# Performance work log

Measured on AMD Instinct MI355X. Metric: run time of the kernel, lower is better.

## Reference

```python
import jax, jax.numpy as jnp
import numpy as np

C_IN = 256
K = 4
C_QK = C_IN // K  # 64


def setup_inputs() -> dict:
    key = jax.random.key(0)
    ks = jax.random.split(key, 9)
    B, C, H, W = 4, C_IN, 64, 64
    s = 0.02
    return {
        "x": jax.random.normal(ks[0], (B, C, H, W), dtype=jnp.float32),
        # 1x1 convs stored as dense [out, in] matrices (kernel_size=1)
        "wq": jax.random.normal(ks[1], (C_QK, C), dtype=jnp.float32) * s,
        "bq": jax.random.normal(ks[2], (C_QK,), dtype=jnp.float32) * s,
        "wk": jax.random.normal(ks[3], (C_QK, C), dtype=jnp.float32) * s,
        "bk": jax.random.normal(ks[4], (C_QK,), dtype=jnp.float32) * s,
        "wv": jax.random.normal(ks[5], (C, C), dtype=jnp.float32) * s,
        "bv": jax.random.normal(ks[6], (C,), dtype=jnp.float32) * s,
        "wg": jax.random.normal(ks[7], (C, C), dtype=jnp.float32) * s,
        "bg": jax.random.normal(ks[8], (C,), dtype=jnp.float32) * s,
    }


def reference(x, wq, bq, wk, bk, wv, bv, wg, bg):
    B, C, H, W = x.shape
    N = H * W
    xf = x.reshape(B, C, N)  # [B, C, N]
    # 1x1 conv == per-pixel linear over channels
    q = jnp.einsum("oc,bcn->bon", wq, xf) + bq[None, :, None]  # [B, Cqk, N]
    k = jnp.einsum("oc,bcn->bon", wk, xf) + bk[None, :, None]  # [B, Cqk, N]
    v = jnp.einsum("oc,bcn->bon", wv, xf) + bv[None, :, None]  # [B, C, N]
    # energy[b, n, m] = <q[:, n], k[:, m]>  (n = query pos, m = key pos)
    energy = jnp.einsum("bon,bom->bnm", q, k)  # [B, N, N]
    energy = jax.nn.elu(energy) / N
    # out[b, c, m] = sum_n v[b, c, n] * energy[b, n, m]
    out = jnp.einsum("bcn,bnm->bcm", v, energy).reshape(B, C, H, W)
    out = jnp.einsum("oc,bchw->bohw", wg, out) + bg[None, :, None, None]
    return out
```

## Files before the change

### kernel.cpp

```cpp
#include <hip/hip_runtime.h>

#define B_ 4
#define C_ 256
#define CQK 64
#define N_ 4096
#define SEG 2
#define SEGN (N_ / SEG)
#define NB 128
#define ITERS (SEGN / NB)
#define TS 512

typedef _Float16 f16;
typedef __attribute__((ext_vector_type(8))) _Float16 f16x8;
typedef __attribute__((ext_vector_type(4))) _Float16 f16x4;
typedef __attribute__((ext_vector_type(4))) float f32x4;
typedef __attribute__((ext_vector_type(4))) float float4v;

#define TILE_OFF(l15, quad) ((l15) * 32 + (quad) * 8)

__global__ __launch_bounds__(256) void prep_w(
    const float* __restrict__ wq, const float* __restrict__ wk,
    const float* __restrict__ wv, const float* __restrict__ wg,
    f16* __restrict__ WQt, f16* __restrict__ WKt, f16* __restrict__ WVt,
    f16* __restrict__ WGt) {
  int chunk = blockIdx.x * 256 + threadIdx.x;
  if (chunk >= 20480) return;
  const float* src;
  f16* dst;
  int lo;
  if (chunk < 2048) { src = wq; dst = WQt; lo = chunk * 8; }
  else if (chunk < 4096) { src = wk; dst = WKt; lo = (chunk - 2048) * 8; }
  else if (chunk < 12288) { src = wv; dst = WVt; lo = (chunk - 4096) * 8; }
  else { src = wg; dst = WGt; lo = (chunk - 12288) * 8; }
  int o = lo >> 8, k = lo & 255;
  f16x8 v;
#pragma unroll
  for (int j = 0; j < 8; j++) v[j] = (f16)src[lo + j];
  *(f16x8*)(dst + ((size_t)(o >> 4) * 8 + (k >> 5)) * TS + (o & 15) * 32 + (k & 31)) = v;
}

__global__ __launch_bounds__(512) void proj(
    const float* __restrict__ x, const f16* __restrict__ WQt,
    const f16* __restrict__ WKt, const f16* __restrict__ WVt,
    const float* __restrict__ bq, const float* __restrict__ bk,
    const float* __restrict__ bv, f16* __restrict__ QTt, f16* __restrict__ KTt,
    f16* __restrict__ Vt) {
  __shared__ float xs[64][65];
  __shared__ f16 xt[4 * 8 * TS];
  int n0 = blockIdx.x * 64;
  int b = blockIdx.y;
  int tid = threadIdx.x, lane = tid & 63, w = tid >> 6;
  int l15 = lane & 15, quad = lane >> 4;
  const float* xb = x + (size_t)b * C_ * N_;

  for (int cc = 0; cc < 4; cc++) {
#pragma unroll
    for (int i = 0; i < 8; i++)
      xs[lane][w * 8 + i] = xb[(size_t)(cc * 64 + w * 8 + i) * N_ + n0 + lane];
    __syncthreads();
    {
      int nt = w >> 1;
      f16x8 v;
#pragma unroll
      for (int j = 0; j < 8; j++)
        v[j] = (f16)xs[nt * 16 + l15][32 * (w & 1) + quad * 8 + j];
      *(f16x8*)(xt + (nt * 8 + cc * 2 + (w & 1)) * TS + l15 * 32 + quad * 8) = v;
    }
    __syncthreads();
  }

  f32x4 acc[3][4];
#pragma unroll
  for (int j = 0; j < 3; j++)
#pragma unroll
    for (int nt = 0; nt < 4; nt++) acc[j][nt] = (f32x4){0.f, 0.f, 0.f, 0.f};

#pragma unroll
  for (int kt = 0; kt < 8; kt++) {
    f16x8 xf[4];
#pragma unroll
    for (int nt = 0; nt < 4; nt++)
      xf[nt] = *(const f16x8*)(xt + (nt * 8 + kt) * TS + TILE_OFF(l15, quad));
#pragma unroll
    for (int j = 0; j < 3; j++) {
      int g = w * 3 + j;
      const f16* Wt;
      int ot;
      bool isV = g < 16;
      if (isV) { Wt = WVt; ot = g; }
      else if (g < 20) { Wt = WQt; ot = g - 16; }
      else { Wt = WKt; ot = g - 20; }
      f16x8 wf = *(const f16x8*)(Wt + ((size_t)ot * 8 + kt) * TS + TILE_OFF(l15, quad));
#pragma unroll
      for (int nt = 0; nt < 4; nt++)
        acc[j][nt] = isV
            ? __builtin_amdgcn_mfma_f32_16x16x32_f16(xf[nt], wf, acc[j][nt], 0, 0, 0)
            : __builtin_amdgcn_mfma_f32_16x16x32_f16(wf, xf[nt], acc[j][nt], 0, 0, 0);
    }
  }

  f16* vbout = Vt + (size_t)b * C_ * N_;
#pragma unroll
  for (int j = 0; j < 3; j++) {
    int g = w * 3 + j;
    if (g < 16) {
      float bvv = bv[16 * g + l15];
#pragma unroll
      for (int nt = 0; nt < 4; nt++) {
        f16x4 vals;
#pragma unroll
        for (int r = 0; r < 4; r++) vals[r] = (f16)(acc[j][nt][r] + bvv);
        *(f16x4*)(vbout + ((size_t)g * 128 + (n0 >> 5) + (nt >> 1)) * TS +
                  l15 * 32 + 16 * (nt & 1) + 4 * quad) = vals;
      }
    } else {
      int oq = (g < 20) ? (g - 16) : (g - 20);
      const float* bias = (g < 20) ? bq : bk;
      f16* ob = ((g < 20) ? QTt : KTt) + (size_t)b * N_ * CQK;
#pragma unroll
      for (int nt = 0; nt < 4; nt++) {
        f16x4 vals;
#pragma unroll
        for (int r = 0; r < 4; r++)
          vals[r] = (f16)(acc[j][nt][r] + bias[16 * oq + 4 * quad + r]);
        *(f16x4*)(ob + (((size_t)(n0 >> 4) + nt) * 2 + (oq >> 1)) * TS + l15 * 32 +
                  16 * (oq & 1) + 4 * quad) = vals;
      }
    }
  }
}

__global__ __launch_bounds__(256, 2) void attn(const f16* __restrict__ qt,
                                               const f16* __restrict__ kt,
                                               const f16* __restrict__ v,
                                               const f16* __restrict__ WGt,
                                               f16* __restrict__ part) {
  __shared__ __align__(16) f16 sPt[2][64][128];
  int sb = blockIdx.x;
  int seg = sb >> 2;
  int b = sb & 3;
  int m0 = blockIdx.y * 64;
  int tid = threadIdx.x, lane = tid & 63, w = tid >> 6;
  int l15 = lane & 15, quad = lane >> 4;
  const f16* qtb = qt + (size_t)b * N_ * CQK;
  const f16* ktb = kt + (size_t)b * N_ * CQK;
  const f16* vb = v + (size_t)b * C_ * N_;

  f32x4 oacc[4][4];
#pragma unroll
  for (int ct = 0; ct < 4; ct++)
#pragma unroll
    for (int mt = 0; mt < 4; mt++) oacc[ct][mt] = (f32x4){0.f, 0.f, 0.f, 0.f};

  f16x8 kf[4][2];
#pragma unroll
  for (int mt = 0; mt < 4; mt++)
#pragma unroll
    for (int ks = 0; ks < 2; ks++)
      kf[mt][ks] = *(const f16x8*)(ktb + ((size_t)((m0 >> 4) + mt) * 2 + ks) * TS +
                                   TILE_OFF(l15, quad));

  f16x8 qf[2][2];
  {
    int nq = seg * SEGN;
#pragma unroll
    for (int nt = 0; nt < 2; nt++)
#pragma unroll
      for (int ks = 0; ks < 2; ks++)
        qf[nt][ks] = *(const f16x8*)(qtb +
                                     ((size_t)((nq >> 4) + 2 * w + nt) * 2 + ks) * TS +
                                     TILE_OFF(l15, quad));
  }

  for (int it = 0; it < ITERS; it++) {
    int n0 = seg * SEGN + it * NB;
    f16x8 vfA[2][4];
#pragma unroll
    for (int ks = 0; ks < 2; ks++)
#pragma unroll
      for (int ct = 0; ct < 4; ct++)
        vfA[ks][ct] = *(const f16x8*)(vb +
                                      ((size_t)(4 * w + ct) * 128 + (n0 >> 5) + ks) * TS +
                                      TILE_OFF(l15, quad));

    char* buf = (char*)sPt[it & 1];
#pragma unroll
    for (int nt = 0; nt < 2; nt++) {
      f32x4 sacc[4];
#pragma unroll
      for (int mt = 0; mt < 4; mt++) sacc[mt] = (f32x4){0.f, 0.f, 0.f, 0.f};
#pragma unroll
      for (int ks = 0; ks < 2; ks++)
#pragma unroll
        for (int mt = 0; mt < 4; mt++)
          sacc[mt] = __builtin_amdgcn_mfma_f32_16x16x32_f16(qf[nt][ks], kf[mt][ks],
                                                            sacc[mt], 0, 0, 0);
#pragma unroll
      for (int mt = 0; mt < 4; mt++) {
        f16x4 p;
#pragma unroll
        for (int r = 0; r < 4; r++) {
          float s = sacc[mt][r];
          p[r] = (f16)(s > 0.0f ? s : (__expf(s) - 1.0f));
        }
        int row = 16 * mt + l15;
        int colb = (64 * w + 32 * nt + 8 * quad) ^ ((row & 7) << 4);
        *(f16x4*)(buf + row * 256 + colb) = p;
      }
    }
    __syncthreads();

    f16x8 vfB[2][4];
    f16x8 pa[4];
#pragma unroll
    for (int mt = 0; mt < 4; mt++) {
      int row = 16 * mt + l15;
      pa[mt] = *(const f16x8*)(buf + row * 256 + ((quad * 16) ^ ((row & 7) << 4)));
    }
#pragma unroll
    for (int ks = 0; ks < 2; ks++)
#pragma unroll
      for (int ct = 0; ct < 4; ct++)
        vfB[ks][ct] = *(const f16x8*)(vb + ((size_t)(4 * w + ct) * 128 + (n0 >> 5) +
                                            2 + ks) * TS +
                                      TILE_OFF(l15, quad));
#pragma unroll
    for (int ct = 0; ct < 4; ct++)
#pragma unroll
      for (int mt = 0; mt < 4; mt++)
        oacc[ct][mt] = __builtin_amdgcn_mfma_f32_16x16x32_f16(vfA[0][ct], pa[mt],
                                                              oacc[ct][mt], 0, 0, 0);
    if (it + 1 < ITERS) {
      int nq = n0 + NB;
#pragma unroll
      for (int nt = 0; nt < 2; nt++)
#pragma unroll
        for (int ks = 0; ks < 2; ks++)
          qf[nt][ks] = *(const f16x8*)(qtb +
                                       ((size_t)((nq >> 4) + 2 * w + nt) * 2 + ks) * TS +
                                       TILE_OFF(l15, quad));
    }
#pragma unroll
    for (int mt = 0; mt < 4; mt++) {
      int row = 16 * mt + l15;
      pa[mt] = *(const f16x8*)(buf + row * 256 + ((64 + quad * 16) ^ ((row & 7) << 4)));
    }
#pragma unroll
    for (int ct = 0; ct < 4; ct++)
#pragma unroll
      for (int mt = 0; mt < 4; mt++)
        oacc[ct][mt] = __builtin_amdgcn_mfma_f32_16x16x32_f16(vfA[1][ct], pa[mt],
                                                              oacc[ct][mt], 0, 0, 0);
#pragma unroll
    for (int mt = 0; mt < 4; mt++) {
      int row = 16 * mt + l15;
      pa[mt] = *(const f16x8*)(buf + row * 256 + ((128 + quad * 16) ^ ((row & 7) << 4)));
    }
#pragma unroll
    for (int ct = 0; ct < 4; ct++)
#pragma unroll
      for (int mt = 0; mt < 4; mt++)
        oacc[ct][mt] = __builtin_amdgcn_mfma_f32_16x16x32_f16(vfB[0][ct], pa[mt],
                                                              oacc[ct][mt], 0, 0, 0);
#pragma unroll
    for (int mt = 0; mt < 4; mt++) {
      int row = 16 * mt + l15;
      pa[mt] = *(const f16x8*)(buf + row * 256 + ((192 + quad * 16) ^ ((row & 7) << 4)));
    }
#pragma unroll
    for (int ct = 0; ct < 4; ct++)
#pragma unroll
      for (int mt = 0; mt < 4; mt++)
        oacc[ct][mt] = __builtin_amdgcn_mfma_f32_16x16x32_f16(vfB[1][ct], pa[mt],
                                                              oacc[ct][mt], 0, 0, 0);
  }

  __syncthreads();
  f16* obuf = (f16*)sPt;
#pragma unroll
  for (int ct = 0; ct < 4; ct++) {
#pragma unroll
    for (int mt = 0; mt < 4; mt++) {
      f16x4 vals;
#pragma unroll
      for (int r = 0; r < 4; r++)
        vals[r] = (f16)(oacc[ct][mt][r] * (1.0f / (float)N_));
      *(f16x4*)(obuf + (mt * 8 + 2 * w + (ct >> 1)) * TS + l15 * 32 +
                16 * (ct & 1) + 4 * quad) = vals;
    }
  }
  __syncthreads();
  f32x4 accO[4][4];
#pragma unroll
  for (int ot = 0; ot < 4; ot++)
#pragma unroll
    for (int mt = 0; mt < 4; mt++) accO[ot][mt] = (f32x4){0.f, 0.f, 0.f, 0.f};
#pragma unroll
  for (int kt = 0; kt < 8; kt++) {
    f16x8 bO[4];
#pragma unroll
    for (int mt = 0; mt < 4; mt++)
      bO[mt] = *(const f16x8*)(obuf + (mt * 8 + kt) * TS + TILE_OFF(l15, quad));
#pragma unroll
    for (int ot = 0; ot < 4; ot++) {
      f16x8 af = *(const f16x8*)(WGt + ((size_t)(4 * w + ot) * 8 + kt) * TS +
                                 TILE_OFF(l15, quad));
#pragma unroll
      for (int mt = 0; mt < 4; mt++)
        accO[ot][mt] = __builtin_amdgcn_mfma_f32_16x16x32_f16(af, bO[mt], accO[ot][mt], 0, 0, 0);
    }
  }
  f16* pb = part + ((size_t)(seg * B_ + b) * C_) * N_;
#pragma unroll
  for (int ot = 0; ot < 4; ot++) {
#pragma unroll
    for (int mt = 0; mt < 4; mt++) {
      int m = m0 + 16 * mt + l15;
#pragma unroll
      for (int r = 0; r < 4; r++) {
        int o = 64 * w + 16 * ot + 4 * quad + r;
        pb[(size_t)o * N_ + m] = (f16)accO[ot][mt][r];
      }
    }
  }
}

__global__ __launch_bounds__(256) void combine(const f16* __restrict__ part,
                                               const float* __restrict__ bg,
                                               float* __restrict__ out) {
  size_t i = ((size_t)blockIdx.x * 256 + threadIdx.x) * 8;
  f16x8 p0 = *(const f16x8*)(part + i);
  f16x8 p1 = *(const f16x8*)(part + (size_t)B_ * C_ * N_ + i);
  float bgo = bg[(i >> 12) & 255];
  float4v r0, r1;
#pragma unroll
  for (int j = 0; j < 4; j++) r0[j] = (float)p0[j] + (float)p1[j] + bgo;
#pragma unroll
  for (int j = 0; j < 4; j++) r1[j] = (float)p0[4 + j] + (float)p1[4 + j] + bgo;
  *(float4v*)(out + i) = r0;
  *(float4v*)(out + i + 4) = r1;
}

extern "C" void kernel_launch(void* const* d_in, const int* in_sizes, int n_in,
                              void* d_out, int out_size, void* d_ws, size_t ws_size,
                              hipStream_t stream) {
  const float* x = (const float*)d_in[0];
  const float* wq = (const float*)d_in[1];
  const float* bq = (const float*)d_in[2];
  const float* wk = (const float*)d_in[3];
  const float* bk = (const float*)d_in[4];
  const float* wv = (const float*)d_in[5];
  const float* bv = (const float*)d_in[6];
  const float* wg = (const float*)d_in[7];
  const float* bg = (const float*)d_in[8];
  float* out = (float*)d_out;

  char* ws = (char*)d_ws;
  f16* QTt = (f16*)ws; ws += (size_t)B_ * N_ * CQK * sizeof(f16);
  f16* KTt = (f16*)ws; ws += (size_t)B_ * N_ * CQK * sizeof(f16);
  f16* Vt  = (f16*)ws; ws += (size_t)B_ * C_ * N_ * sizeof(f16);
  f16* WQt = (f16*)ws; ws += (size_t)CQK * C_ * sizeof(f16);
  f16* WKt = (f16*)ws; ws += (size_t)CQK * C_ * sizeof(f16);
  f16* WVt = (f16*)ws; ws += (size_t)C_ * C_ * sizeof(f16);
  f16* WGt = (f16*)ws; ws += (size_t)C_ * C_ * sizeof(f16);
  f16* PART = (f16*)ws; ws += (size_t)SEG * B_ * C_ * N_ * sizeof(f16);

  prep_w<<<dim3(80), 256, 0, stream>>>(wq, wk, wv, wg, WQt, WKt, WVt, WGt);
  proj<<<dim3(N_ / 64, B_), 512, 0, stream>>>(x, WQt, WKt, WVt, bq, bk, bv,
                                              QTt, KTt, Vt);
  attn<<<dim3(8, N_ / 64), 256, 0, stream>>>(QTt, KTt, Vt, WGt, PART);
  combine<<<dim3(2048), 256, 0, stream>>>(PART, bg, out);
}
```

Measured before the change: 160.5 us.

## Split attention block across 8 waves and stage K tile in LDS

The attention kernel now runs with 512 threads (8 waves) per block instead of 256. Each wave handles 16 query rows and 32 channels rather than 32 and 64, which halves per-wave accumulators and register fragments, and launch bounds are raised to target 4 blocks per SM. The K fragments are loaded once into shared memory and re-read from LDS each iteration, where before they were held in registers. This adds LDS traffic and more waves contending at each barrier, in exchange for higher occupancy to hide memory latency.

```diff
diff --git a/kernel.cpp b/kernel.cpp
--- a/kernel.cpp
+++ b/kernel.cpp
@@ -130,11 +130,12 @@
   }
 }
 
-__global__ __launch_bounds__(256, 2) void attn(const f16* __restrict__ qt,
+__global__ __launch_bounds__(512, 4) void attn(const f16* __restrict__ qt,
                                                const f16* __restrict__ kt,
                                                const f16* __restrict__ v,
                                                const f16* __restrict__ WGt,
                                                f16* __restrict__ part) {
+  __shared__ __align__(16) f16 sK[8 * TS];
   __shared__ __align__(16) f16 sPt[2][64][128];
   int sb = blockIdx.x;
   int seg = sb >> 2;
@@ -146,110 +147,98 @@
   const f16* ktb = kt + (size_t)b * N_ * CQK;
   const f16* vb = v + (size_t)b * C_ * N_;
 
-  f32x4 oacc[4][4];
-#pragma unroll
-  for (int ct = 0; ct < 4; ct++)
+  *(f16x8*)(sK + w * TS + TILE_OFF(l15, quad)) =
+      *(const f16x8*)(ktb + ((size_t)((m0 >> 4) + (w >> 1)) * 2 + (w & 1)) * TS +
+                      TILE_OFF(l15, quad));
+
+  f32x4 oacc[2][4];
+#pragma unroll
+  for (int ct = 0; ct < 2; ct++)
 #pragma unroll
     for (int mt = 0; mt < 4; mt++) oacc[ct][mt] = (f32x4){0.f, 0.f, 0.f, 0.f};
 
-  f16x8 kf[4][2];
-#pragma unroll
-  for (int mt = 0; mt < 4; mt++)
-#pragma unroll
-    for (int ks = 0; ks < 2; ks++)
-      kf[mt][ks] = *(const f16x8*)(ktb + ((size_t)((m0 >> 4) + mt) * 2 + ks) * TS +
-                                   TILE_OFF(l15, quad));
-
-  f16x8 qf[2][2];
-  {
-    int nq = seg * SEGN;
-#pragma unroll
-    for (int nt = 0; nt < 2; nt++)
-#pragma unroll
-      for (int ks = 0; ks < 2; ks++)
-        qf[nt][ks] = *(const f16x8*)(qtb +
-                                     ((size_t)((nq >> 4) + 2 * w + nt) * 2 + ks) * TS +
-                                     TILE_OFF(l15, quad));
-  }
+  f16x8 qf[2];
+#pragma unroll
+  for (int ks = 0; ks < 2; ks++)
+    qf[ks] = *(const f16x8*)(qtb + ((size_t)(((seg * SEGN) >> 4) + w) * 2 + ks) * TS +
+                             TILE_OFF(l15, quad));
+
+  __syncthreads();
 
   for (int it = 0; it < ITERS; it++) {
     int n0 = seg * SEGN + it * NB;
-    f16x8 vfA[2][4];
-#pragma unroll
-    for (int ks = 0; ks < 2; ks++)
-#pragma unroll
-      for (int ct = 0; ct < 4; ct++)
-        vfA[ks][ct] = *(const f16x8*)(vb +
-                                      ((size_t)(4 * w + ct) * 128 + (n0 >> 5) + ks) * TS +
-                                      TILE_OFF(l15, quad));
-
     char* buf = (char*)sPt[it & 1];
-#pragma unroll
-    for (int nt = 0; nt < 2; nt++) {
-      f32x4 sacc[4];
-#pragma unroll
-      for (int mt = 0; mt < 4; mt++) sacc[mt] = (f32x4){0.f, 0.f, 0.f, 0.f};
-#pragma unroll
-      for (int ks = 0; ks < 2; ks++)
-#pragma unroll
-        for (int mt = 0; mt < 4; mt++)
-          sacc[mt] = __builtin_amdgcn_mfma_f32_16x16x32_f16(qf[nt][ks], kf[mt][ks],
-                                                            sacc[mt], 0, 0, 0);
-#pragma unroll
-      for (int mt = 0; mt < 4; mt++) {
-        f16x4 p;
-#pragma unroll
-        for (int r = 0; r < 4; r++) {
-          float s = sacc[mt][r];
-          p[r] = (f16)(s > 0.0f ? s : (__expf(s) - 1.0f));
-        }
-        int row = 16 * mt + l15;
-        int colb = (64 * w + 32 * nt + 8 * quad) ^ ((row & 7) << 4);
-        *(f16x4*)(buf + row * 256 + colb) = p;
+
+    f32x4 sacc[4];
+#pragma unroll
+    for (int mt = 0; mt < 4; mt++) sacc[mt] = (f32x4){0.f, 0.f, 0.f, 0.f};
+#pragma unroll
+    for (int ks = 0; ks < 2; ks++) {
+      f16x8 kf[4];
+#pragma unroll
+      for (int mt = 0; mt < 4; mt++)
+        kf[mt] = *(const f16x8*)(sK + (mt * 2 + ks) * TS + TILE_OFF(l15, quad));
+#pragma unroll
+      for (int mt = 0; mt < 4; mt++)
+        sacc[mt] = __builtin_amdgcn_mfma_f32_16x16x32_f16(qf[ks], kf[mt], sacc[mt],
+                                                          0, 0, 0);
+    }
+#pragma unroll
+    for (int mt = 0; mt < 4; mt++) {
+      f16x4 p;
+#pragma unroll
+      for (int r = 0; r < 4; r++) {
+        float s = sacc[mt][r];
+        p[r] = (f16)(s > 0.0f ? s : (__expf(s) - 1.0f));
       }
+      int row = 16 * mt + l15;
+      int colb = (32 * w + 8 * quad) ^ ((row & 7) << 4);
+      *(f16x4*)(buf + row * 256 + colb) = p;
     }
     __syncthreads();
 
-    f16x8 vfB[2][4];
-    f16x8 pa[4];
-#pragma unroll
-    for (int mt = 0; mt < 4; mt++) {
-      int row = 16 * mt + l15;
-      pa[mt] = *(const f16x8*)(buf + row * 256 + ((quad * 16) ^ ((row & 7) << 4)));
-    }
-#pragma unroll
-    for (int ks = 0; ks < 2; ks++)
-#pragma unroll
-      for (int ct = 0; ct < 4; ct++)
-        vfB[ks][ct] = *(const f16x8*)(vb + ((size_t)(4 * w + ct) * 128 + (n0 >> 5) +
-                                            2 + ks) * TS +
-                                      TILE_OFF(l15, quad));
-#pragma unroll
-    for (int ct = 0; ct < 4; ct++)
-#pragma unroll
-      for (int mt = 0; mt < 4; mt++)
-        oacc[ct][mt] = __builtin_amdgcn_mfma_f32_16x16x32_f16(vfA[0][ct], pa[mt],
-                                                              oacc[ct][mt], 0, 0, 0);
     if (it + 1 < ITERS) {
       int nq = n0 + NB;
 #pragma unroll
-      for (int nt = 0; nt < 2; nt++)
-#pragma unroll
-        for (int ks = 0; ks < 2; ks++)
-          qf[nt][ks] = *(const f16x8*)(qtb +
-                                       ((size_t)((nq >> 4) + 2 * w + nt) * 2 + ks) * TS +
-                                       TILE_OFF(l15, quad));
-    }
+      for (int ks = 0; ks < 2; ks++)
+        qf[ks] = *(const f16x8*)(qtb + ((size_t)((nq >> 4) + w) * 2 + ks) * TS +
+                                 TILE_OFF(l15, quad));
+    }
+
+    f16x8 vfa[2], vfb[2], pa[4];
+#pragma unroll
+    for (int ct = 0; ct < 2; ct++)
+      vfa[ct] = *(const f16x8*)(vb + ((size_t)(2 * w + ct) * 128 + (n0 >> 5) + 0) * TS +
+                                TILE_OFF(l15, quad));
+#pragma unroll
+    for (int mt = 0; mt < 4; mt++) {
+      int row = 16 * mt + l15;
+      pa[mt] = *(const f16x8*)(buf + row * 256 + ((0 + quad * 16) ^ ((row & 7) << 4)));
+    }
+#pragma unroll
+    for (int ct = 0; ct < 2; ct++)
+      vfb[ct] = *(const f16x8*)(vb + ((size_t)(2 * w + ct) * 128 + (n0 >> 5) + 1) * TS +
+                                TILE_OFF(l15, quad));
+#pragma unroll
+    for (int ct = 0; ct < 2; ct++)
+#pragma unroll
+      for (int mt = 0; mt < 4; mt++)
+        oacc[ct][mt] = __builtin_amdgcn_mfma_f32_16x16x32_f16(vfa[ct], pa[mt],
+                                                              oacc[ct][mt], 0, 0, 0);
 #pragma unroll
     for (int mt = 0; mt < 4; mt++) {
       int row = 16 * mt + l15;
       pa[mt] = *(const f16x8*)(buf + row * 256 + ((64 + quad * 16) ^ ((row & 7) << 4)));
     }
 #pragma unroll
-    for (int ct = 0; ct < 4; ct++)
-#pragma unroll
-      for (int mt = 0; mt < 4; mt++)
-        oacc[ct][mt] = __builtin_amdgcn_mfma_f32_16x16x32_f16(vfA[1][ct], pa[mt],
+    for (int ct = 0; ct < 2; ct++)
+      vfa[ct] = *(const f16x8*)(vb + ((size_t)(2 * w + ct) * 128 + (n0 >> 5) + 2) * TS +
+                                TILE_OFF(l15, quad));
+#pragma unroll
+    for (int ct = 0; ct < 2; ct++)
+#pragma unroll
+      for (int mt = 0; mt < 4; mt++)
+        oacc[ct][mt] = __builtin_amdgcn_mfma_f32_16x16x32_f16(vfb[ct], pa[mt],
                                                               oacc[ct][mt], 0, 0, 0);
 #pragma unroll
     for (int mt = 0; mt < 4; mt++) {
@@ -257,10 +246,14 @@
       pa[mt] = *(const f16x8*)(buf + row * 256 + ((128 + quad * 16) ^ ((row & 7) << 4)));
     }
 #pragma unroll
-    for (int ct = 0; ct < 4; ct++)
-#pragma unroll
-      for (int mt = 0; mt < 4; mt++)
-        oacc[ct][mt] = __builtin_amdgcn_mfma_f32_16x16x32_f16(vfB[0][ct], pa[mt],
+    for (int ct = 0; ct < 2; ct++)
+      vfb[ct] = *(const f16x8*)(vb + ((size_t)(2 * w + ct) * 128 + (n0 >> 5) + 3) * TS +
+                                TILE_OFF(l15, quad));
+#pragma unroll
+    for (int ct = 0; ct < 2; ct++)
+#pragma unroll
+      for (int mt = 0; mt < 4; mt++)
+        oacc[ct][mt] = __builtin_amdgcn_mfma_f32_16x16x32_f16(vfa[ct], pa[mt],
                                                               oacc[ct][mt], 0, 0, 0);
 #pragma unroll
     for (int mt = 0; mt < 4; mt++) {
@@ -268,31 +261,30 @@
       pa[mt] = *(const f16x8*)(buf + row * 256 + ((192 + quad * 16) ^ ((row & 7) << 4)));
     }
 #pragma unroll
-    for (int ct = 0; ct < 4; ct++)
-#pragma unroll
-      for (int mt = 0; mt < 4; mt++)
-        oacc[ct][mt] = __builtin_amdgcn_mfma_f32_16x16x32_f16(vfB[1][ct], pa[mt],
+    for (int ct = 0; ct < 2; ct++)
+#pragma unroll
+      for (int mt = 0; mt < 4; mt++)
+        oacc[ct][mt] = __builtin_amdgcn_mfma_f32_16x16x32_f16(vfb[ct], pa[mt],
                                                               oacc[ct][mt], 0, 0, 0);
   }
 
   __syncthreads();
   f16* obuf = (f16*)sPt;
 #pragma unroll
-  for (int ct = 0; ct < 4; ct++) {
+  for (int ct = 0; ct < 2; ct++) {
 #pragma unroll
     for (int mt = 0; mt < 4; mt++) {
       f16x4 vals;
 #pragma unroll
       for (int r = 0; r < 4; r++)
         vals[r] = (f16)(oacc[ct][mt][r] * (1.0f / (float)N_));
-      *(f16x4*)(obuf + (mt * 8 + 2 * w + (ct >> 1)) * TS + l15 * 32 +
-                16 * (ct & 1) + 4 * quad) = vals;
+      *(f16x4*)(obuf + (mt * 8 + w) * TS + l15 * 32 + 16 * ct + 4 * quad) = vals;
     }
   }
   __syncthreads();
-  f32x4 accO[4][4];
-#pragma unroll
-  for (int ot = 0; ot < 4; ot++)
+  f32x4 accO[2][4];
+#pragma unroll
+  for (int ot = 0; ot < 2; ot++)
 #pragma unroll
     for (int mt = 0; mt < 4; mt++) accO[ot][mt] = (f32x4){0.f, 0.f, 0.f, 0.f};
 #pragma unroll
@@ -302,23 +294,24 @@
     for (int mt = 0; mt < 4; mt++)
       bO[mt] = *(const f16x8*)(obuf + (mt * 8 + kt) * TS + TILE_OFF(l15, quad));
 #pragma unroll
-    for (int ot = 0; ot < 4; ot++) {
-      f16x8 af = *(const f16x8*)(WGt + ((size_t)(4 * w + ot) * 8 + kt) * TS +
+    for (int ot = 0; ot < 2; ot++) {
+      f16x8 af = *(const f16x8*)(WGt + ((size_t)(2 * w + ot) * 8 + kt) * TS +
                                  TILE_OFF(l15, quad));
 #pragma unroll
       for (int mt = 0; mt < 4; mt++)
-        accO[ot][mt] = __builtin_amdgcn_mfma_f32_16x16x32_f16(af, bO[mt], accO[ot][mt], 0, 0, 0);
+        accO[ot][mt] = __builtin_amdgcn_mfma_f32_16x16x32_f16(af, bO[mt], accO[ot][mt],
+                                                              0, 0, 0);
     }
   }
   f16* pb = part + ((size_t)(seg * B_ + b) * C_) * N_;
 #pragma unroll
-  for (int ot = 0; ot < 4; ot++) {
+  for (int ot = 0; ot < 2; ot++) {
 #pragma unroll
     for (int mt = 0; mt < 4; mt++) {
       int m = m0 + 16 * mt + l15;
 #pragma unroll
       for (int r = 0; r < 4; r++) {
-        int o = 64 * w + 16 * ot + 4 * quad + r;
+        int o = 32 * w + 16 * ot + 4 * quad + r;
         pb[(size_t)o * N_ + m] = (f16)accO[ot][mt][r];
       }
     }
@@ -368,6 +361,6 @@
   prep_w<<<dim3(80), 256, 0, stream>>>(wq, wk, wv, wg, WQt, WKt, WVt, WGt);
   proj<<<dim3(N_ / 64, B_), 512, 0, stream>>>(x, WQt, WKt, WVt, bq, bk, bv,
                                               QTt, KTt, Vt);
-  attn<<<dim3(8, N_ / 64), 256, 0, stream>>>(QTt, KTt, Vt, WGt, PART);
+  attn<<<dim3(SEG * B_, N_ / 64), 512, 0, stream>>>(QTt, KTt, Vt, WGt, PART);
   combine<<<dim3(2048), 256, 0, stream>>>(PART, bg, out);
 }
```

Result: no change. 160.4 us (-0.0%).

## Fuse split-N combine into attention via float atomics and stagger iteration order

Applied to the files above, without the earlier changes.

Drops the fp16 partial buffer and the separate combine kernel. Each attention block now atomically adds its fp32 projected result, plus half the bias, straight into the zeroed output. It also rotates the starting N-iteration per block so concurrent blocks read different V/Q tiles and spread cache and channel traffic. This trades a write-and-reread of partials and one launch for a memset and scattered, uncoalesced atomic adds.

```diff
diff --git a/kernel.cpp b/kernel.cpp
--- a/kernel.cpp
+++ b/kernel.cpp
@@ -134,12 +134,14 @@
                                                const f16* __restrict__ kt,
                                                const f16* __restrict__ v,
                                                const f16* __restrict__ WGt,
-                                               f16* __restrict__ part) {
+                                               const float* __restrict__ bg,
+                                               float* __restrict__ out) {
   __shared__ __align__(16) f16 sPt[2][64][128];
   int sb = blockIdx.x;
   int seg = sb >> 2;
   int b = sb & 3;
   int m0 = blockIdx.y * 64;
+  int it0 = ((((int)blockIdx.y >> 5) << 3) ^ (((int)blockIdx.y & 7) << 1)) & (ITERS - 1);
   int tid = threadIdx.x, lane = tid & 63, w = tid >> 6;
   int l15 = lane & 15, quad = lane >> 4;
   const f16* qtb = qt + (size_t)b * N_ * CQK;
@@ -162,7 +164,7 @@
 
   f16x8 qf[2][2];
   {
-    int nq = seg * SEGN;
+    int nq = seg * SEGN + it0 * NB;
 #pragma unroll
     for (int nt = 0; nt < 2; nt++)
 #pragma unroll
@@ -172,7 +174,8 @@
                                      TILE_OFF(l15, quad));
   }
 
-  for (int it = 0; it < ITERS; it++) {
+  for (int i = 0; i < ITERS; i++) {
+    int it = (i + it0) & (ITERS - 1);
     int n0 = seg * SEGN + it * NB;
     f16x8 vfA[2][4];
 #pragma unroll
@@ -183,7 +186,7 @@
                                       ((size_t)(4 * w + ct) * 128 + (n0 >> 5) + ks) * TS +
                                       TILE_OFF(l15, quad));
 
-    char* buf = (char*)sPt[it & 1];
+    char* buf = (char*)sPt[i & 1];
 #pragma unroll
     for (int nt = 0; nt < 2; nt++) {
       f32x4 sacc[4];
@@ -230,8 +233,9 @@
       for (int mt = 0; mt < 4; mt++)
         oacc[ct][mt] = __builtin_amdgcn_mfma_f32_16x16x32_f16(vfA[0][ct], pa[mt],
                                                               oacc[ct][mt], 0, 0, 0);
-    if (it + 1 < ITERS) {
-      int nq = n0 + NB;
+    if (i + 1 < ITERS) {
+      int itn = (i + 1 + it0) & (ITERS - 1);
+      int nq = seg * SEGN + itn * NB;
 #pragma unroll
       for (int nt = 0; nt < 2; nt++)
 #pragma unroll
@@ -310,35 +314,21 @@
         accO[ot][mt] = __builtin_amdgcn_mfma_f32_16x16x32_f16(af, bO[mt], accO[ot][mt], 0, 0, 0);
     }
   }
-  f16* pb = part + ((size_t)(seg * B_ + b) * C_) * N_;
+  float* ob = out + (size_t)b * C_ * N_;
 #pragma unroll
   for (int ot = 0; ot < 4; ot++) {
+    float4v bgq = *(const float4v*)(bg + 64 * w + 16 * ot + 4 * quad);
 #pragma unroll
     for (int mt = 0; mt < 4; mt++) {
       int m = m0 + 16 * mt + l15;
 #pragma unroll
       for (int r = 0; r < 4; r++) {
         int o = 64 * w + 16 * ot + 4 * quad + r;
-        pb[(size_t)o * N_ + m] = (f16)accO[ot][mt][r];
+        atomicAdd(&ob[(size_t)o * N_ + m],
+                  accO[ot][mt][r] + bgq[r] * (1.0f / (float)SEG));
       }
     }
   }
-}
-
-__global__ __launch_bounds__(256) void combine(const f16* __restrict__ part,
-                                               const float* __restrict__ bg,
-                                               float* __restrict__ out) {
-  size_t i = ((size_t)blockIdx.x * 256 + threadIdx.x) * 8;
-  f16x8 p0 = *(const f16x8*)(part + i);
-  f16x8 p1 = *(const f16x8*)(part + (size_t)B_ * C_ * N_ + i);
-  float bgo = bg[(i >> 12) & 255];
-  float4v r0, r1;
-#pragma unroll
-  for (int j = 0; j < 4; j++) r0[j] = (float)p0[j] + (float)p1[j] + bgo;
-#pragma unroll
-  for (int j = 0; j < 4; j++) r1[j] = (float)p0[4 + j] + (float)p1[4 + j] + bgo;
-  *(float4v*)(out + i) = r0;
-  *(float4v*)(out + i + 4) = r1;
 }
 
 extern "C" void kernel_launch(void* const* d_in, const int* in_sizes, int n_in,
@@ -363,11 +353,10 @@
   f16* WKt = (f16*)ws; ws += (size_t)CQK * C_ * sizeof(f16);
   f16* WVt = (f16*)ws; ws += (size_t)C_ * C_ * sizeof(f16);
   f16* WGt = (f16*)ws; ws += (size_t)C_ * C_ * sizeof(f16);
-  f16* PART = (f16*)ws; ws += (size_t)SEG * B_ * C_ * N_ * sizeof(f16);
-
+
+  hipMemsetAsync(out, 0, out_size, stream);
   prep_w<<<dim3(80), 256, 0, stream>>>(wq, wk, wv, wg, WQt, WKt, WVt, WGt);
   proj<<<dim3(N_ / 64, B_), 512, 0, stream>>>(x, WQt, WKt, WVt, bq, bk, bv,
                                               QTt, KTt, Vt);
-  attn<<<dim3(8, N_ / 64), 256, 0, stream>>>(QTt, KTt, Vt, WGt, PART);
-  combine<<<dim3(2048), 256, 0, stream>>>(PART, bg, out);
+  attn<<<dim3(SEG * B_, N_ / 64), 256, 0, stream>>>(QTt, KTt, Vt, WGt, bg, out);
 }
```

Measured after the change: 171.7 us. 7.0% more time.

## Software-pipeline attention: compute next tile's ELU scores during current PV MFMAs

Applied to the files above, without the earlier changes.

Restructures the attention loop so the QK^T score MFMAs and ELU for the next key block are interleaved with the PV accumulation MFMAs of the current block, writing into the alternate LDS buffer. A prologue computes the first score tile, and the single barrier per iteration moves to the loop end. This targets the serialization between score computation, the barrier and the PV matmul, at the cost of extra live registers (s0/s1) that may reduce occupancy or cause spills.

```diff
diff --git a/kernel.cpp b/kernel.cpp
--- a/kernel.cpp
+++ b/kernel.cpp
@@ -161,29 +161,16 @@
                                    TILE_OFF(l15, quad));
 
   f16x8 qf[2][2];
+#pragma unroll
+  for (int nt = 0; nt < 2; nt++)
+#pragma unroll
+    for (int ks = 0; ks < 2; ks++)
+      qf[nt][ks] = *(const f16x8*)(qtb +
+                                   ((size_t)(((seg * SEGN) >> 4) + 2 * w + nt) * 2 + ks) * TS +
+                                   TILE_OFF(l15, quad));
+
   {
-    int nq = seg * SEGN;
-#pragma unroll
-    for (int nt = 0; nt < 2; nt++)
-#pragma unroll
-      for (int ks = 0; ks < 2; ks++)
-        qf[nt][ks] = *(const f16x8*)(qtb +
-                                     ((size_t)((nq >> 4) + 2 * w + nt) * 2 + ks) * TS +
-                                     TILE_OFF(l15, quad));
-  }
-
-  for (int it = 0; it < ITERS; it++) {
-    int n0 = seg * SEGN + it * NB;
-    f16x8 vfA[2][4];
-#pragma unroll
-    for (int ks = 0; ks < 2; ks++)
-#pragma unroll
-      for (int ct = 0; ct < 4; ct++)
-        vfA[ks][ct] = *(const f16x8*)(vb +
-                                      ((size_t)(4 * w + ct) * 128 + (n0 >> 5) + ks) * TS +
-                                      TILE_OFF(l15, quad));
-
-    char* buf = (char*)sPt[it & 1];
+    char* buf = (char*)sPt[0];
 #pragma unroll
     for (int nt = 0; nt < 2; nt++) {
       f32x4 sacc[4];
@@ -208,15 +195,60 @@
         *(f16x4*)(buf + row * 256 + colb) = p;
       }
     }
-    __syncthreads();
+  }
+  {
+    int nq = seg * SEGN + NB;
+#pragma unroll
+    for (int nt = 0; nt < 2; nt++)
+#pragma unroll
+      for (int ks = 0; ks < 2; ks++)
+        qf[nt][ks] = *(const f16x8*)(qtb +
+                                     ((size_t)((nq >> 4) + 2 * w + nt) * 2 + ks) * TS +
+                                     TILE_OFF(l15, quad));
+  }
+  __syncthreads();
+
+  for (int it = 0; it < ITERS; it++) {
+    int n0 = seg * SEGN + it * NB;
+    char* rbuf = (char*)sPt[it & 1];
+    char* wbuf = (char*)sPt[(it + 1) & 1];
+    bool hasNext = (it + 1 < ITERS);
+
+    f16x8 vfA[2][4];
+#pragma unroll
+    for (int ks = 0; ks < 2; ks++)
+#pragma unroll
+      for (int ct = 0; ct < 4; ct++)
+        vfA[ks][ct] = *(const f16x8*)(vb +
+                                      ((size_t)(4 * w + ct) * 128 + (n0 >> 5) + ks) * TS +
+                                      TILE_OFF(l15, quad));
+
+    f32x4 s0[4], s1[4];
+    if (hasNext) {
+#pragma unroll
+      for (int mt = 0; mt < 4; mt++) s0[mt] = (f32x4){0.f, 0.f, 0.f, 0.f};
+#pragma unroll
+      for (int ks = 0; ks < 2; ks++)
+#pragma unroll
+        for (int mt = 0; mt < 4; mt++)
+          s0[mt] = __builtin_amdgcn_mfma_f32_16x16x32_f16(qf[0][ks], kf[mt][ks],
+                                                          s0[mt], 0, 0, 0);
+    }
+
+    f16x8 pa[4];
+#pragma unroll
+    for (int mt = 0; mt < 4; mt++) {
+      int row = 16 * mt + l15;
+      pa[mt] = *(const f16x8*)(rbuf + row * 256 + ((quad * 16) ^ ((row & 7) << 4)));
+    }
+#pragma unroll
+    for (int ct = 0; ct < 4; ct++)
+#pragma unroll
+      for (int mt = 0; mt < 4; mt++)
+        oacc[ct][mt] = __builtin_amdgcn_mfma_f32_16x16x32_f16(vfA[0][ct], pa[mt],
+                                                              oacc[ct][mt], 0, 0, 0);
 
     f16x8 vfB[2][4];
-    f16x8 pa[4];
-#pragma unroll
-    for (int mt = 0; mt < 4; mt++) {
-      int row = 16 * mt + l15;
-      pa[mt] = *(const f16x8*)(buf + row * 256 + ((quad * 16) ^ ((row & 7) << 4)));
-    }
 #pragma unroll
     for (int ks = 0; ks < 2; ks++)
 #pragma unroll
@@ -224,26 +256,26 @@
         vfB[ks][ct] = *(const f16x8*)(vb + ((size_t)(4 * w + ct) * 128 + (n0 >> 5) +
                                             2 + ks) * TS +
                                       TILE_OFF(l15, quad));
-#pragma unroll
-    for (int ct = 0; ct < 4; ct++)
-#pragma unroll
-      for (int mt = 0; mt < 4; mt++)
-        oacc[ct][mt] = __builtin_amdgcn_mfma_f32_16x16x32_f16(vfA[0][ct], pa[mt],
-                                                              oacc[ct][mt], 0, 0, 0);
-    if (it + 1 < ITERS) {
-      int nq = n0 + NB;
-#pragma unroll
-      for (int nt = 0; nt < 2; nt++)
-#pragma unroll
-        for (int ks = 0; ks < 2; ks++)
-          qf[nt][ks] = *(const f16x8*)(qtb +
-                                       ((size_t)((nq >> 4) + 2 * w + nt) * 2 + ks) * TS +
-                                       TILE_OFF(l15, quad));
-    }
+
+    if (hasNext) {
+#pragma unroll
+      for (int mt = 0; mt < 4; mt++) {
+        f16x4 p;
+#pragma unroll
+        for (int r = 0; r < 4; r++) {
+          float s = s0[mt][r];
+          p[r] = (f16)(s > 0.0f ? s : (__expf(s) - 1.0f));
+        }
+        int row = 16 * mt + l15;
+        int colb = (64 * w + 8 * quad) ^ ((row & 7) << 4);
+        *(f16x4*)(wbuf + row * 256 + colb) = p;
+      }
+    }
+
 #pragma unroll
     for (int mt = 0; mt < 4; mt++) {
       int row = 16 * mt + l15;
-      pa[mt] = *(const f16x8*)(buf + row * 256 + ((64 + quad * 16) ^ ((row & 7) << 4)));
+      pa[mt] = *(const f16x8*)(rbuf + row * 256 + ((64 + quad * 16) ^ ((row & 7) << 4)));
     }
 #pragma unroll
     for (int ct = 0; ct < 4; ct++)
@@ -251,10 +283,22 @@
       for (int mt = 0; mt < 4; mt++)
         oacc[ct][mt] = __builtin_amdgcn_mfma_f32_16x16x32_f16(vfA[1][ct], pa[mt],
                                                               oacc[ct][mt], 0, 0, 0);
+
+    if (hasNext) {
+#pragma unroll
+      for (int mt = 0; mt < 4; mt++) s1[mt] = (f32x4){0.f, 0.f, 0.f, 0.f};
+#pragma unroll
+      for (int ks = 0; ks < 2; ks++)
+#pragma unroll
+        for (int mt = 0; mt < 4; mt++)
+          s1[mt] = __builtin_amdgcn_mfma_f32_16x16x32_f16(qf[1][ks], kf[mt][ks],
+                                                          s1[mt], 0, 0, 0);
+    }
+
 #pragma unroll
     for (int mt = 0; mt < 4; mt++) {
       int row = 16 * mt + l15;
-      pa[mt] = *(const f16x8*)(buf + row * 256 + ((128 + quad * 16) ^ ((row & 7) << 4)));
+      pa[mt] = *(const f16x8*)(rbuf + row * 256 + ((128 + quad * 16) ^ ((row & 7) << 4)));
     }
 #pragma unroll
     for (int ct = 0; ct < 4; ct++)
@@ -262,10 +306,36 @@
       for (int mt = 0; mt < 4; mt++)
         oacc[ct][mt] = __builtin_amdgcn_mfma_f32_16x16x32_f16(vfB[0][ct], pa[mt],
                                                               oacc[ct][mt], 0, 0, 0);
+
+    if (hasNext) {
+#pragma unroll
+      for (int mt = 0; mt < 4; mt++) {
+        f16x4 p;
+#pragma unroll
+        for (int r = 0; r < 4; r++) {
+          float s = s1[mt][r];
+          p[r] = (f16)(s > 0.0f ? s : (__expf(s) - 1.0f));
+        }
+        int row = 16 * mt + l15;
+        int colb = (64 * w + 32 + 8 * quad) ^ ((row & 7) << 4);
+        *(f16x4*)(wbuf + row * 256 + colb) = p;
+      }
+      if (it + 2 < ITERS) {
+        int nq = seg * SEGN + (it + 2) * NB;
+#pragma unroll
+        for (int nt = 0; nt < 2; nt++)
+#pragma unroll
+          for (int ks = 0; ks < 2; ks++)
+            qf[nt][ks] = *(const f16x8*)(qtb +
+                                         ((size_t)((nq >> 4) + 2 * w + nt) * 2 + ks) * TS +
+                                         TILE_OFF(l15, quad));
+      }
+    }
+
 #pragma unroll
     for (int mt = 0; mt < 4; mt++) {
       int row = 16 * mt + l15;
-      pa[mt] = *(const f16x8*)(buf + row * 256 + ((192 + quad * 16) ^ ((row & 7) << 4)));
+      pa[mt] = *(const f16x8*)(rbuf + row * 256 + ((192 + quad * 16) ^ ((row & 7) << 4)));
     }
 #pragma unroll
     for (int ct = 0; ct < 4; ct++)
@@ -273,9 +343,10 @@
       for (int mt = 0; mt < 4; mt++)
         oacc[ct][mt] = __builtin_amdgcn_mfma_f32_16x16x32_f16(vfB[1][ct], pa[mt],
                                                               oacc[ct][mt], 0, 0, 0);
-  }
-
-  __syncthreads();
+
+    __syncthreads();
+  }
+
   f16* obuf = (f16*)sPt;
 #pragma unroll
   for (int ct = 0; ct < 4; ct++) {
@@ -368,6 +439,6 @@
   prep_w<<<dim3(80), 256, 0, stream>>>(wq, wk, wv, wg, WQt, WKt, WVt, WGt);
   proj<<<dim3(N_ / 64, B_), 512, 0, stream>>>(x, WQt, WKt, WVt, bq, bk, bv,
                                               QTt, KTt, Vt);
-  attn<<<dim3(8, N_ / 64), 256, 0, stream>>>(QTt, KTt, Vt, WGt, PART);
+  attn<<<dim3(SEG * B_, N_ / 64), 256, 0, stream>>>(QTt, KTt, Vt, WGt, PART);
   combine<<<dim3(2048), 256, 0, stream>>>(PART, bg, out);
 }
```

Result: faster. 157.3 us, median of 2 (-2.0%).
